# Performance work log

Hardware: AMD Instinct MI355X
Metric: run time of the kernel (lower is better)

The kernel has to match this reference:

```python
import jax, jax.numpy as jnp
import numpy as np

B, T, S, D, H = 32, 256, 256, 512, 1024
VNT, VR = 300, 20000


def setup_inputs() -> dict:
    key = jax.random.key(0)
    ks = jax.random.split(key, 18)
    s = 0.02  # weight init scale to keep tanh/sigmoid unsaturated
    inp = {}
    inp['nt'] = jax.random.randint(ks[0], (B, T), 0, VNT)
    inp['prev_rules'] = jax.random.randint(ks[1], (B, T), 0, VR)
    inp['parent_rules'] = jax.random.randint(ks[2], (B, T), 0, VR)
    # parent timestep for each position; values >= i fall back to initial zero state slot
    inp['parent_t'] = jax.random.randint(ks[3], (B, T), 0, T)
    inp['context'] = jax.random.normal(ks[4], (B, S, H), jnp.float32)
    inp['context_lengths'] = jax.random.randint(ks[5], (B,), 1, S + 1)
    inp['h0'] = jnp.zeros((B, H), jnp.float32)
    inp['c0'] = jnp.zeros((B, H), jnp.float32)
    # embedding tables; row 0 is padding_idx -> zeroed
    inp['nt_emb'] = (jax.random.normal(ks[6], (VNT, D), jnp.float32)).at[0].set(0.0)
    inp['rule_emb'] = (jax.random.normal(ks[7], (VR, D), jnp.float32)).at[0].set(0.0)
    IN = 3 * D + H
    inp['W_ih'] = jax.random.normal(ks[8], (4 * H, IN), jnp.float32) * s
    inp['W_hh'] = jax.random.normal(ks[9], (4 * H, H), jnp.float32) * s
    inp['b_ih'] = jnp.zeros((4 * H,), jnp.float32)
    inp['b_hh'] = jnp.zeros((4 * H,), jnp.float32)
    inp['Wa_in'] = jax.random.normal(ks[10], (H, H), jnp.float32) * s
    inp['Wa_out'] = jax.random.normal(ks[11], (H, 2 * H), jnp.float32) * s
    inp['Wc_in'] = jax.random.normal(ks[12], (H, H), jnp.float32) * s
    inp['Wc_out'] = jax.random.normal(ks[13], (H, 2 * H), jnp.float32) * s
    return inp


def _forward(nt, prev_rules, parent_rules, parent_t, context, context_lengths,
             h0, c0, nt_emb, rule_emb, W_ih, W_hh, b_ih, b_hh,
             Wa_in, Wa_out, Wc_in, Wc_out):
    Bv, Tv = nt.shape
    Sv = context.shape[1]
    Hv = h0.shape[-1]
    dt = context.dtype

    nt_e = nt_emb[nt]               # [B,T,D]
    rule_e = rule_emb[prev_rules]   # [B,T,D]
    par_e = rule_emb[parent_rules]  # [B,T,D]

    src_mask = jnp.arange(Sv)[None, :] < context_lengths[:, None]  # [B,S]
    neg_inf = jnp.finfo(dt).min

    def global_attn(q, W_in, W_out):
        # OpenNMT GlobalAttention, attn_type='general', single decode step
        scores = jnp.einsum('bh,bsh->bs', q @ W_in.T, context)
        scores = jnp.where(src_mask, scores, neg_inf)
        p = jax.nn.softmax(scores, axis=-1)                 # [B,S]
        c_vec = jnp.einsum('bs,bsh->bh', p, context)        # [B,H]
        out = jnp.tanh(jnp.concatenate([c_vec, q], axis=-1) @ W_out.T)
        return out, p

    def step(carry, xs):
        h, c, buf, i = carry
        nt_i, r_i, pr_i, pidx = xs
        # gather parent hidden state; future/invalid parent -> slot 0 (initial zeros)
        idx = jnp.where(pidx < i, pidx + 1, 0)                       # [B]
        pstate = jnp.take_along_axis(buf, idx[:, None, None], axis=1)[:, 0]  # [B,H]
        x = jnp.concatenate([nt_i, r_i, pr_i, pstate], axis=-1)     # [B,3D+H]
        gates = x @ W_ih.T + h @ W_hh.T + b_ih + b_hh
        ig, fg, gg, og = jnp.split(gates, 4, axis=-1)                # torch order i,f,g,o
        c_new = jax.nn.sigmoid(fg) * c + jax.nn.sigmoid(ig) * jnp.tanh(gg)
        h_new = jax.nn.sigmoid(og) * jnp.tanh(c_new)
        a_out, a_p = global_attn(h_new, Wa_in, Wa_out)
        _, cp_p = global_attn(a_out, Wc_in, Wc_out)
        # scatter this step's rnn output into the parent-state buffer (slot i+1)
        buf = buf.at[:, i + 1, :].set(h_new)
        return (h_new, c_new, buf, i + 1), (a_out, a_p, cp_p)

    buf0 = jnp.zeros((Bv, Tv + 1, Hv), dt)
    xs = (nt_e.swapaxes(0, 1), rule_e.swapaxes(0, 1), par_e.swapaxes(0, 1),
          parent_t.swapaxes(0, 1))
    _, (outs, att, cp) = jax.lax.scan(step, (h0, c0, buf0, jnp.int32(0)), xs)
    output = outs.swapaxes(0, 1)       # [B,T,H]
    attn_scores = att.swapaxes(0, 1)   # [B,T,S]
    copy_scores = cp.swapaxes(0, 1)    # [B,T,S]
    return output, attn_scores, copy_scores


def reference(nt, prev_rules, parent_rules, parent_t, context, context_lengths,
              h0, c0, nt_emb, rule_emb, W_ih, W_hh, b_ih, b_hh,
              Wa_in, Wa_out, Wc_in, Wc_out):
    return _forward(nt, prev_rules, parent_rules, parent_t, context,
                    context_lengths, h0, c0, nt_emb, rule_emb, W_ih, W_hh,
                    b_ih, b_hh, Wa_in, Wa_out, Wc_in, Wc_out)
```

## Files before the change

kernel.cpp:

```cpp
#include <hip/hip_runtime.h>

typedef _Float16 f16;
typedef _Float16 h8 __attribute__((ext_vector_type(8)));
typedef float f4 __attribute__((ext_vector_type(4)));

#define Bn 32
#define Tn 256
#define Sn 256
#define Hn 1024
#define INn 2560
#define KT 3584
#define SW_PAD 3592
#define SLOT 32832

__device__ __forceinline__ f4 mfma_f16(h8 a, h8 b, f4 c) {
  return __builtin_amdgcn_mfma_f32_16x16x32_f16(a, b, c, 0, 0, 0);
}
__device__ __forceinline__ float sigm(float x) { return 1.0f / (1.0f + __expf(-x)); }

__global__ void k_prep_weights(const float* __restrict__ W_ih, const float* __restrict__ W_hh,
                               const float* __restrict__ Wa_in, const float* __restrict__ Wc_in,
                               const float* __restrict__ Wa_out, const float* __restrict__ b_ih,
                               const float* __restrict__ b_hh,
                               f16* __restrict__ Wcomb, f16* __restrict__ Wain,
                               f16* __restrict__ Wcin, f16* __restrict__ Waout,
                               float* __restrict__ bcomb) {
  long idx = (long)blockIdx.x * 256 + threadIdx.x;
  if (idx < 14680064L) {
    int n = (int)(idx / KT), k = (int)(idx % KT);
    float v = (k < INn) ? W_ih[(long)n * INn + k] : W_hh[(long)n * Hn + (k - INn)];
    Wcomb[idx] = (f16)v;
    return;
  }
  idx -= 14680064L;
  if (idx < 1048576) { Wain[idx] = (f16)Wa_in[idx]; return; }
  idx -= 1048576;
  if (idx < 1048576) { Wcin[idx] = (f16)Wc_in[idx]; return; }
  idx -= 1048576;
  if (idx < 2097152) { Waout[idx] = (f16)Wa_out[idx]; return; }
  idx -= 2097152;
  if (idx < 4096) bcomb[idx] = b_ih[idx] + b_hh[idx];
}

__global__ void k_prep_ctx(const float* __restrict__ context,
                           f16* __restrict__ ctx16, f16* __restrict__ ctxT) {
  int idx = blockIdx.x * 256 + threadIdx.x;
  int b = idx >> 18;
  int rem = idx & 262143;
  int s = rem >> 10, k = rem & 1023;
  float v = context[idx];
  ctx16[idx] = (f16)v;
  ctxT[((long)b << 18) + ((long)k << 8) + s] = (f16)v;
}

__global__ void k_prep_xemb(const int* __restrict__ nt, const int* __restrict__ prev_r,
                            const int* __restrict__ par_r,
                            const float* __restrict__ nt_emb, const float* __restrict__ rule_emb,
                            f16* __restrict__ xemb) {
  int bt = blockIdx.x;
  int b = bt >> 8, t = bt & 255;
  int nti = nt[bt], pri = prev_r[bt], pai = par_r[bt];
  f16* dst = xemb + ((long)t * Bn + b) * 1536;
  for (int k = threadIdx.x; k < 1536; k += 256) {
    float v;
    if (k < 512)       v = nt_emb[(long)nti * 512 + k];
    else if (k < 1024) v = rule_emb[(long)pri * 512 + (k - 512)];
    else               v = rule_emb[(long)pai * 512 + (k - 1024)];
    dst[k] = (f16)v;
  }
}

__global__ void k_prep_state(f16* __restrict__ bufh, int* __restrict__ flags) {
  int idx = blockIdx.x * 256 + threadIdx.x;
  if (idx < 16384) {
    __hip_atomic_store((unsigned int*)bufh + idx, 0u, __ATOMIC_RELAXED,
                       __HIP_MEMORY_SCOPE_SYSTEM);
  } else {
    __hip_atomic_store(flags + (idx - 16384), 0, __ATOMIC_RELAXED,
                       __HIP_MEMORY_SCOPE_SYSTEM);
  }
}

struct GatesArgs {
  const f16* xemb; const f16* Wcomb; f16* bufh; const float* bcomb;
  const float* c0; const int* parent_t; int* flags;
};

__global__ void __launch_bounds__(512, 1) k_gates(GatesArgs a) {
  const int jt = blockIdx.x;
  const int tid = threadIdx.x;
  const int wave = tid >> 6;
  const int lane = tid & 63;
  const int l15 = lane & 15, quad = lane >> 4;

  extern __shared__ char smem[];
  f16 (*sW)[SW_PAD] = (f16(*)[SW_PAD])smem;
  float* sC    = (float*)(smem + 114944);
  float* sBias = (float*)(smem + 123136);
  float* c_lds = (float*)(smem + 123200);
  f16*   sH    = (f16*)(smem + 123712);
  int*   spidx = (int*)(smem + 123968);

  for (int i = tid; i < 16 * 448; i += 512) {
    int n = i / 448, kk = (i % 448) * 8;
    int gr = (n >> 2) * Hn + jt * 4 + (n & 3);
    *(h8*)&sW[n][kk] = *(const h8*)(a.Wcomb + (long)gr * KT + kk);
  }
  if (tid < 16) sBias[tid] = a.bcomb[(tid >> 2) * Hn + jt * 4 + (tid & 3)];
  if (tid < 128) c_lds[tid] = a.c0[(tid >> 2) * Hn + jt * 4 + (tid & 3)];
  __syncthreads();

  for (int t = 0; t < Tn; ++t) {
    if (tid < 32) {
      int pt = a.parent_t[tid * Tn + t];
      spidx[tid] = (pt < t) ? pt + 1 : 0;
    }

    const f16* xr0 = a.xemb + ((long)t * Bn + l15) * 1536;
    const f16* xr1 = xr0 + 16 * 1536;
    f4 acc0 = (f4){0.f, 0.f, 0.f, 0.f}, acc1 = (f4){0.f, 0.f, 0.f, 0.f};
#pragma unroll
    for (int ks = 0; ks < 6; ++ks) {
      int k = wave * 192 + ks * 32 + quad * 8;
      h8 a0 = *(const h8*)(xr0 + k);
      h8 a1 = *(const h8*)(xr1 + k);
      h8 bf = *(const h8*)&sW[l15][k];
      acc0 = mfma_f16(a0, bf, acc0);
      acc1 = mfma_f16(a1, bf, acc1);
    }

    if (t > 0 && wave == 0) {
      bool ok = false;
      do {
        int f0 = __hip_atomic_load(&a.flags[(lane * 4 + 0) * 32], __ATOMIC_RELAXED, __HIP_MEMORY_SCOPE_SYSTEM);
        int f1 = __hip_atomic_load(&a.flags[(lane * 4 + 1) * 32], __ATOMIC_RELAXED, __HIP_MEMORY_SCOPE_SYSTEM);
        int f2 = __hip_atomic_load(&a.flags[(lane * 4 + 2) * 32], __ATOMIC_RELAXED, __HIP_MEMORY_SCOPE_SYSTEM);
        int f3 = __hip_atomic_load(&a.flags[(lane * 4 + 3) * 32], __ATOMIC_RELAXED, __HIP_MEMORY_SCOPE_SYSTEM);
        ok = (f0 >= t) && (f1 >= t) && (f2 >= t) && (f3 >= t);
      } while (!__all(ok));
    }
    __syncthreads();

    const f16* b0;
    const f16* b1;
    int koff;
    if (wave < 4) {
      int pidx0 = spidx[l15], pidx1 = spidx[16 + l15];
      b0 = a.bufh + (long)pidx0 * SLOT + (long)l15 * 1024;
      b1 = a.bufh + (long)pidx1 * SLOT + (long)(16 + l15) * 1024;
      koff = 1536;
    } else {
      b0 = a.bufh + (long)t * SLOT + (long)l15 * 1024;
      b1 = a.bufh + (long)t * SLOT + (long)(16 + l15) * 1024;
      koff = 2560;
    }
#pragma unroll
    for (int ks = 0; ks < 8; ++ks) {
      int k = 1536 + wave * 256 + ks * 32 + quad * 8;
      h8 a0 = *(const h8*)(b0 + (k - koff));
      h8 a1 = *(const h8*)(b1 + (k - koff));
      h8 bf = *(const h8*)&sW[l15][k];
      acc0 = mfma_f16(a0, bf, acc0);
      acc1 = mfma_f16(a1, bf, acc1);
    }

    float* myC0 = sC + (((wave & 3) * 2 + 0) * 16 + quad * 4) * 16 + l15;
    float* myC1 = sC + (((wave & 3) * 2 + 1) * 16 + quad * 4) * 16 + l15;
    if (wave < 4) {
#pragma unroll
      for (int r = 0; r < 4; ++r) { myC0[r * 16] = acc0[r]; myC1[r * 16] = acc1[r]; }
    }
    __syncthreads();
    if (wave >= 4) {
#pragma unroll
      for (int r = 0; r < 4; ++r) { myC0[r * 16] += acc0[r]; myC1[r * 16] += acc1[r]; }
    }
    __syncthreads();

    if (tid < 128) {
      int b = tid >> 2, jj = tid & 3;
      int mt = b >> 4, row = b & 15;
      float g0 = 0.f, g1 = 0.f, g2 = 0.f, g3 = 0.f;
#pragma unroll
      for (int w = 0; w < 4; ++w) {
        const float* base = sC + ((w * 2 + mt) * 16 + row) * 16 + jj;
        g0 += base[0]; g1 += base[4]; g2 += base[8]; g3 += base[12];
      }
      g0 += sBias[jj]; g1 += sBias[4 + jj]; g2 += sBias[8 + jj]; g3 += sBias[12 + jj];
      float cp = c_lds[tid];
      float cn = sigm(g1) * cp + sigm(g0) * tanhf(g2);
      float hn = sigm(g3) * tanhf(cn);
      c_lds[tid] = cn;
      sH[tid] = (f16)hn;
    }
    __syncthreads();

    if (tid < 32) {
      unsigned long long v = *(const unsigned long long*)(sH + tid * 4);
      __hip_atomic_store((unsigned long long*)(a.bufh + (long)(t + 1) * SLOT
                                               + (long)tid * 1024 + jt * 4),
                         v, __ATOMIC_RELAXED, __HIP_MEMORY_SCOPE_SYSTEM);
    }
    asm volatile("s_waitcnt vmcnt(0)" ::: "memory");
    if (tid == 0)
      __hip_atomic_store(&a.flags[blockIdx.x * 32], t + 1,
                         __ATOMIC_RELAXED, __HIP_MEMORY_SCOPE_SYSTEM);
  }
}

__global__ void k_qgemm(const f16* __restrict__ A, const f16* __restrict__ W,
                        f16* __restrict__ out, int a_mode) {
  int tid = threadIdx.x, lane = tid & 63, wave = tid >> 6;
  int l15 = lane & 15, quad = lane >> 4;
  int wm = wave & 1, wn = wave >> 1;
  int bm = blockIdx.y * 64 + wm * 32, bn = blockIdx.x * 64 + wn * 32;

  const f16* arow[2]; const f16* brow[2];
#pragma unroll
  for (int i = 0; i < 2; ++i) {
    int m = bm + i * 16 + l15;
    arow[i] = a_mode ? A + (long)((m & 255) + 1) * SLOT + (long)(m >> 8) * 1024
                     : A + (long)m * 1024;
  }
#pragma unroll
  for (int j = 0; j < 2; ++j) brow[j] = W + (long)(bn + j * 16 + l15) * 1024;

  f4 acc[2][2];
#pragma unroll
  for (int i = 0; i < 2; ++i)
#pragma unroll
    for (int j = 0; j < 2; ++j) acc[i][j] = (f4){0.f, 0.f, 0.f, 0.f};

  for (int ks = 0; ks < 32; ++ks) {
    int k = ks * 32 + quad * 8;
    h8 af[2] = {*(const h8*)(arow[0] + k), *(const h8*)(arow[1] + k)};
    h8 bf[2] = {*(const h8*)(brow[0] + k), *(const h8*)(brow[1] + k)};
#pragma unroll
    for (int i = 0; i < 2; ++i)
#pragma unroll
      for (int j = 0; j < 2; ++j) acc[i][j] = mfma_f16(af[i], bf[j], acc[i][j]);
  }
#pragma unroll
  for (int i = 0; i < 2; ++i)
#pragma unroll
    for (int j = 0; j < 2; ++j)
#pragma unroll
      for (int r = 0; r < 4; ++r) {
        int m = bm + i * 16 + quad * 4 + r;
        int n = bn + j * 16 + l15;
        out[(long)m * 1024 + n] = (f16)acc[i][j][r];
      }
}

__global__ void k_scores(const f16* __restrict__ Q, const f16* __restrict__ C16,
                         float* __restrict__ outp) {
  int tid = threadIdx.x, lane = tid & 63, wave = tid >> 6;
  int l15 = lane & 15, quad = lane >> 4;
  int wm = wave & 1, wn = wave >> 1;
  int b = blockIdx.z;
  int bm = blockIdx.y * 64 + wm * 32, bn = blockIdx.x * 64 + wn * 32;
  const f16* A = Q + (long)b * 256 * 1024;
  const f16* Bp = C16 + (long)b * 256 * 1024;
  const f16* arow[2]; const f16* brow[2];
#pragma unroll
  for (int i = 0; i < 2; ++i) arow[i] = A + (long)(bm + i * 16 + l15) * 1024;
#pragma unroll
  for (int j = 0; j < 2; ++j) brow[j] = Bp + (long)(bn + j * 16 + l15) * 1024;
  f4 acc[2][2];
#pragma unroll
  for (int i = 0; i < 2; ++i)
#pragma unroll
    for (int j = 0; j < 2; ++j) acc[i][j] = (f4){0.f, 0.f, 0.f, 0.f};
  for (int ks = 0; ks < 32; ++ks) {
    int k = ks * 32 + quad * 8;
    h8 af[2] = {*(const h8*)(arow[0] + k), *(const h8*)(arow[1] + k)};
    h8 bf[2] = {*(const h8*)(brow[0] + k), *(const h8*)(brow[1] + k)};
#pragma unroll
    for (int i = 0; i < 2; ++i)
#pragma unroll
      for (int j = 0; j < 2; ++j) acc[i][j] = mfma_f16(af[i], bf[j], acc[i][j]);
  }
#pragma unroll
  for (int i = 0; i < 2; ++i)
#pragma unroll
    for (int j = 0; j < 2; ++j)
#pragma unroll
      for (int r = 0; r < 4; ++r) {
        int m = bm + i * 16 + quad * 4 + r;
        int n = bn + j * 16 + l15;
        outp[((long)b * 256 + m) * 256 + n] = acc[i][j][r];
      }
}

__global__ void k_softmax(float* __restrict__ rows, const int* __restrict__ ctx_len,
                          f16* __restrict__ pout) {
  int tid = threadIdx.x;
  long base = (long)blockIdx.x * 256;
  int b = blockIdx.x >> 8;
  int len = ctx_len[b];
  float v = rows[base + tid];
  bool valid = tid < len;
  __shared__ float red[256];
  red[tid] = valid ? v : -3.0e38f;
  __syncthreads();
  for (int o = 128; o > 0; o >>= 1) {
    if (tid < o) red[tid] = fmaxf(red[tid], red[tid + o]);
    __syncthreads();
  }
  float m = red[0];
  __syncthreads();
  float e = valid ? __expf(v - m) : 0.f;
  red[tid] = e;
  __syncthreads();
  for (int o = 128; o > 0; o >>= 1) {
    if (tid < o) red[tid] += red[tid + o];
    __syncthreads();
  }
  float p = e / red[0];
  rows[base + tid] = p;
  if (pout) pout[base + tid] = (f16)p;
}

__global__ void k_cvec(const f16* __restrict__ P, const f16* __restrict__ CT,
                       f16* __restrict__ out) {
  int tid = threadIdx.x, lane = tid & 63, wave = tid >> 6;
  int l15 = lane & 15, quad = lane >> 4;
  int wm = wave & 1, wn = wave >> 1;
  int b = blockIdx.z;
  int bm = blockIdx.y * 64 + wm * 32, bn = blockIdx.x * 64 + wn * 32;
  const f16* A = P + (long)b * 256 * 256;
  const f16* Bp = CT + (long)b * 1024 * 256;
  const f16* arow[2]; const f16* brow[2];
#pragma unroll
  for (int i = 0; i < 2; ++i) arow[i] = A + (long)(bm + i * 16 + l15) * 256;
#pragma unroll
  for (int j = 0; j < 2; ++j) brow[j] = Bp + (long)(bn + j * 16 + l15) * 256;
  f4 acc[2][2];
#pragma unroll
  for (int i = 0; i < 2; ++i)
#pragma unroll
    for (int j = 0; j < 2; ++j) acc[i][j] = (f4){0.f, 0.f, 0.f, 0.f};
  for (int ks = 0; ks < 8; ++ks) {
    int k = ks * 32 + quad * 8;
    h8 af[2] = {*(const h8*)(arow[0] + k), *(const h8*)(arow[1] + k)};
    h8 bf[2] = {*(const h8*)(brow[0] + k), *(const h8*)(brow[1] + k)};
#pragma unroll
    for (int i = 0; i < 2; ++i)
#pragma unroll
      for (int j = 0; j < 2; ++j) acc[i][j] = mfma_f16(af[i], bf[j], acc[i][j]);
  }
#pragma unroll
  for (int i = 0; i < 2; ++i)
#pragma unroll
    for (int j = 0; j < 2; ++j)
#pragma unroll
      for (int r = 0; r < 4; ++r) {
        int m = bm + i * 16 + quad * 4 + r;
        int n = bn + j * 16 + l15;
        out[((long)b * 256 + m) * 1024 + n] = (f16)acc[i][j][r];
      }
}

__global__ void k_aout(const f16* __restrict__ CV, const f16* __restrict__ bufh,
                       const f16* __restrict__ W, float* __restrict__ outf,
                       f16* __restrict__ outh) {
  int tid = threadIdx.x, lane = tid & 63, wave = tid >> 6;
  int l15 = lane & 15, quad = lane >> 4;
  int wm = wave & 1, wn = wave >> 1;
  int bm = blockIdx.y * 64 + wm * 32, bn = blockIdx.x * 64 + wn * 32;
  const f16* arow1[2]; const f16* arow2[2]; const f16* brow[2];
#pragma unroll
  for (int i = 0; i < 2; ++i) {
    int m = bm + i * 16 + l15;
    arow1[i] = CV + (long)m * 1024;
    arow2[i] = bufh + (long)((m & 255) + 1) * SLOT + (long)(m >> 8) * 1024;
  }
#pragma unroll
  for (int j = 0; j < 2; ++j) brow[j] = W + (long)(bn + j * 16 + l15) * 2048;
  f4 acc[2][2];
#pragma unroll
  for (int i = 0; i < 2; ++i)
#pragma unroll
    for (int j = 0; j < 2; ++j) acc[i][j] = (f4){0.f, 0.f, 0.f, 0.f};
  for (int ks = 0; ks < 64; ++ks) {
    int k = ks * 32 + quad * 8;
    h8 af[2], bf[2];
    if (k < 1024) {
      af[0] = *(const h8*)(arow1[0] + k);
      af[1] = *(const h8*)(arow1[1] + k);
    } else {
      af[0] = *(const h8*)(arow2[0] + (k - 1024));
      af[1] = *(const h8*)(arow2[1] + (k - 1024));
    }
    bf[0] = *(const h8*)(brow[0] + k);
    bf[1] = *(const h8*)(brow[1] + k);
#pragma unroll
    for (int i = 0; i < 2; ++i)
#pragma unroll
      for (int j = 0; j < 2; ++j) acc[i][j] = mfma_f16(af[i], bf[j], acc[i][j]);
  }
#pragma unroll
  for (int i = 0; i < 2; ++i)
#pragma unroll
    for (int j = 0; j < 2; ++j)
#pragma unroll
      for (int r = 0; r < 4; ++r) {
        int m = bm + i * 16 + quad * 4 + r;
        int n = bn + j * 16 + l15;
        float v = tanhf(acc[i][j][r]);
        outf[(long)m * 1024 + n] = v;
        outh[(long)m * 1024 + n] = (f16)v;
      }
}

extern "C" void kernel_launch(void* const* d_in, const int* in_sizes, int n_in,
                              void* d_out, int out_size, void* d_ws, size_t ws_size,
                              hipStream_t stream) {
  const int*   nt        = (const int*)d_in[0];
  const int*   prev_r    = (const int*)d_in[1];
  const int*   par_r     = (const int*)d_in[2];
  const int*   parent_t  = (const int*)d_in[3];
  const float* context   = (const float*)d_in[4];
  const int*   ctx_len   = (const int*)d_in[5];
  const float* c0        = (const float*)d_in[7];
  const float* nt_emb    = (const float*)d_in[8];
  const float* rule_emb  = (const float*)d_in[9];
  const float* W_ih      = (const float*)d_in[10];
  const float* W_hh      = (const float*)d_in[11];
  const float* b_ih      = (const float*)d_in[12];
  const float* b_hh      = (const float*)d_in[13];
  const float* Wa_in     = (const float*)d_in[14];
  const float* Wa_out    = (const float*)d_in[15];
  const float* Wc_in     = (const float*)d_in[16];
  float* out = (float*)d_out;

  char* ws = (char*)d_ws;
  f16*   bufh  = (f16*)(ws);
  f16*   xemb  = (f16*)(ws + 16875648L);
  f16*   Wcomb = (f16*)(ws + 42041472L);
  f16*   Wain  = (f16*)(ws + 71401600L);
  f16*   Wcin  = (f16*)(ws + 73498752L);
  f16*   Waout = (f16*)(ws + 75595904L);
  f16*   ctx16 = (f16*)(ws + 79790208L);
  f16*   ctxT  = (f16*)(ws + 96567424L);
  f16*   qbuf  = (f16*)(ws + 113344640L);
  f16*   pbuf  = (f16*)(ws + 130121856L);
  f16*   cvec  = (f16*)(ws + 134316160L);
  f16*   aout16= (f16*)(ws + 151093376L);
  int*   flags = (int*)(ws + 167870592L);
  float* bcomb = (float*)(ws + 167903360L);

  float* attn_out = out + 8388608;
  float* copy_out = out + 10485760;

  hipLaunchKernelGGL(k_prep_weights, dim3(73744), dim3(256), 0, stream,
                     W_ih, W_hh, Wa_in, Wc_in, Wa_out, b_ih, b_hh,
                     Wcomb, Wain, Wcin, Waout, bcomb);
  hipLaunchKernelGGL(k_prep_ctx, dim3(32768), dim3(256), 0, stream, context, ctx16, ctxT);
  hipLaunchKernelGGL(k_prep_xemb, dim3(8192), dim3(256), 0, stream,
                     nt, prev_r, par_r, nt_emb, rule_emb, xemb);
  hipLaunchKernelGGL(k_prep_state, dim3(96), dim3(256), 0, stream, bufh, flags);

  GatesArgs ga{xemb, Wcomb, bufh, bcomb, c0, parent_t, flags};
  void* gp[] = {&ga};
  hipLaunchCooperativeKernel((void*)k_gates, dim3(256), dim3(512), gp, 124096, stream);

  hipLaunchKernelGGL(k_qgemm, dim3(16, 128), dim3(256), 0, stream, bufh, Wain, qbuf, 1);
  hipLaunchKernelGGL(k_scores, dim3(4, 4, 32), dim3(256), 0, stream, qbuf, ctx16, attn_out);
  hipLaunchKernelGGL(k_softmax, dim3(8192), dim3(256), 0, stream, attn_out, ctx_len, pbuf);
  hipLaunchKernelGGL(k_cvec, dim3(16, 4, 32), dim3(256), 0, stream, pbuf, ctxT, cvec);
  hipLaunchKernelGGL(k_aout, dim3(16, 128), dim3(256), 0, stream, cvec, bufh, Waout, out, aout16);
  hipLaunchKernelGGL(k_qgemm, dim3(16, 128), dim3(256), 0, stream, aout16, Wcin, qbuf, 0);
  hipLaunchKernelGGL(k_scores, dim3(4, 4, 32), dim3(256), 0, stream, qbuf, ctx16, copy_out);
  hipLaunchKernelGGL(k_softmax, dim3(8192), dim3(256), 0, stream, copy_out, ctx_len, (f16*)nullptr);
}
```

Measured before the change: 3.007 ms.

## Use a hierarchical gather-broadcast grid barrier and pad LDS gate scratch

The per-timestep grid barrier in the persistent LSTM gates kernel is restructured. Per-block flags are now packed contiguously instead of strided by 32 ints. Block 0 alone polls all 256 flags, then publishes the step number to 8 epoch slots, and every other block spins on a single slot. The aim is to cut the global polling traffic of 256 blocks each reading 256 flags on every step, at the cost of an extra gather-then-broadcast hop on the critical path and more write contention on the shared flag cache lines. Separately, the gate-sum LDS scratch gets a row stride of 17 to reduce bank conflicts.

```diff
diff --git a/kernel.cpp b/kernel.cpp
--- a/kernel.cpp
+++ b/kernel.cpp
@@ -12,6 +12,7 @@
 #define KT 3584
 #define SW_PAD 3592
 #define SLOT 32832
+#define SC_PAD 17
 
 __device__ __forceinline__ f4 mfma_f16(h8 a, h8 b, f4 c) {
   return __builtin_amdgcn_mfma_f32_16x16x32_f16(a, b, c, 0, 0, 0);
@@ -75,7 +76,7 @@
   if (idx < 16384) {
     __hip_atomic_store((unsigned int*)bufh + idx, 0u, __ATOMIC_RELAXED,
                        __HIP_MEMORY_SCOPE_SYSTEM);
-  } else {
+  } else if (idx < 16384 + 640) {
     __hip_atomic_store(flags + (idx - 16384), 0, __ATOMIC_RELAXED,
                        __HIP_MEMORY_SCOPE_SYSTEM);
   }
@@ -96,10 +97,10 @@
   extern __shared__ char smem[];
   f16 (*sW)[SW_PAD] = (f16(*)[SW_PAD])smem;
   float* sC    = (float*)(smem + 114944);
-  float* sBias = (float*)(smem + 123136);
-  float* c_lds = (float*)(smem + 123200);
-  f16*   sH    = (f16*)(smem + 123712);
-  int*   spidx = (int*)(smem + 123968);
+  float* sBias = (float*)(smem + 123648);
+  float* c_lds = (float*)(smem + 123712);
+  f16*   sH    = (f16*)(smem + 124224);
+  int*   spidx = (int*)(smem + 124480);
 
   for (int i = tid; i < 16 * 448; i += 512) {
     int n = i / 448, kk = (i % 448) * 8;
@@ -130,14 +131,25 @@
     }
 
     if (t > 0 && wave == 0) {
-      bool ok = false;
-      do {
-        int f0 = __hip_atomic_load(&a.flags[(lane * 4 + 0) * 32], __ATOMIC_RELAXED, __HIP_MEMORY_SCOPE_SYSTEM);
-        int f1 = __hip_atomic_load(&a.flags[(lane * 4 + 1) * 32], __ATOMIC_RELAXED, __HIP_MEMORY_SCOPE_SYSTEM);
-        int f2 = __hip_atomic_load(&a.flags[(lane * 4 + 2) * 32], __ATOMIC_RELAXED, __HIP_MEMORY_SCOPE_SYSTEM);
-        int f3 = __hip_atomic_load(&a.flags[(lane * 4 + 3) * 32], __ATOMIC_RELAXED, __HIP_MEMORY_SCOPE_SYSTEM);
-        ok = (f0 >= t) && (f1 >= t) && (f2 >= t) && (f3 >= t);
-      } while (!__all(ok));
+      if (jt == 0) {
+        bool ok = false;
+        do {
+          int f0 = __hip_atomic_load(&a.flags[lane],       __ATOMIC_RELAXED, __HIP_MEMORY_SCOPE_SYSTEM);
+          int f1 = __hip_atomic_load(&a.flags[64 + lane],  __ATOMIC_RELAXED, __HIP_MEMORY_SCOPE_SYSTEM);
+          int f2 = __hip_atomic_load(&a.flags[128 + lane], __ATOMIC_RELAXED, __HIP_MEMORY_SCOPE_SYSTEM);
+          int f3 = __hip_atomic_load(&a.flags[192 + lane], __ATOMIC_RELAXED, __HIP_MEMORY_SCOPE_SYSTEM);
+          ok = (f0 >= t) && (f1 >= t) && (f2 >= t) && (f3 >= t);
+        } while (!__all(ok));
+        if (lane < 8)
+          __hip_atomic_store(&a.flags[512 + lane * 16], t,
+                             __ATOMIC_RELAXED, __HIP_MEMORY_SCOPE_SYSTEM);
+      } else {
+        const int ei = 512 + ((jt & 7) << 4);
+        int e;
+        do {
+          e = __hip_atomic_load(&a.flags[ei], __ATOMIC_RELAXED, __HIP_MEMORY_SCOPE_SYSTEM);
+        } while (e < t);
+      }
     }
     __syncthreads();
 
@@ -164,16 +176,16 @@
       acc1 = mfma_f16(a1, bf, acc1);
     }
 
-    float* myC0 = sC + (((wave & 3) * 2 + 0) * 16 + quad * 4) * 16 + l15;
-    float* myC1 = sC + (((wave & 3) * 2 + 1) * 16 + quad * 4) * 16 + l15;
+    float* myC0 = sC + (((wave & 3) * 2 + 0) * 16 + quad * 4) * SC_PAD + l15;
+    float* myC1 = sC + (((wave & 3) * 2 + 1) * 16 + quad * 4) * SC_PAD + l15;
     if (wave < 4) {
 #pragma unroll
-      for (int r = 0; r < 4; ++r) { myC0[r * 16] = acc0[r]; myC1[r * 16] = acc1[r]; }
+      for (int r = 0; r < 4; ++r) { myC0[r * SC_PAD] = acc0[r]; myC1[r * SC_PAD] = acc1[r]; }
     }
     __syncthreads();
     if (wave >= 4) {
 #pragma unroll
-      for (int r = 0; r < 4; ++r) { myC0[r * 16] += acc0[r]; myC1[r * 16] += acc1[r]; }
+      for (int r = 0; r < 4; ++r) { myC0[r * SC_PAD] += acc0[r]; myC1[r * SC_PAD] += acc1[r]; }
     }
     __syncthreads();
 
@@ -183,7 +195,7 @@
       float g0 = 0.f, g1 = 0.f, g2 = 0.f, g3 = 0.f;
 #pragma unroll
       for (int w = 0; w < 4; ++w) {
-        const float* base = sC + ((w * 2 + mt) * 16 + row) * 16 + jj;
+        const float* base = sC + ((w * 2 + mt) * 16 + row) * SC_PAD + jj;
         g0 += base[0]; g1 += base[4]; g2 += base[8]; g3 += base[12];
       }
       g0 += sBias[jj]; g1 += sBias[4 + jj]; g2 += sBias[8 + jj]; g3 += sBias[12 + jj];
@@ -203,7 +215,7 @@
     }
     asm volatile("s_waitcnt vmcnt(0)" ::: "memory");
     if (tid == 0)
-      __hip_atomic_store(&a.flags[blockIdx.x * 32], t + 1,
+      __hip_atomic_store(&a.flags[jt], t + 1,
                          __ATOMIC_RELAXED, __HIP_MEMORY_SCOPE_SYSTEM);
   }
 }
@@ -463,7 +475,7 @@
 
   GatesArgs ga{xemb, Wcomb, bufh, bcomb, c0, parent_t, flags};
   void* gp[] = {&ga};
-  hipLaunchCooperativeKernel((void*)k_gates, dim3(256), dim3(512), gp, 124096, stream);
+  hipLaunchCooperativeKernel((void*)k_gates, dim3(256), dim3(512), gp, 124608, stream);
 
   hipLaunchKernelGGL(k_qgemm, dim3(16, 128), dim3(256), 0, stream, bufh, Wain, qbuf, 1);
   hipLaunchKernelGGL(k_scores, dim3(4, 4, 32), dim3(256), 0, stream, qbuf, ctx16, attn_out);
```

After: 2.932 ms. 1.03x faster.
